# Kernel optimization log

Measured on AMD Instinct MI355X. Metric: run time of the kernel, lower is better.

The kernel has to match this reference:

```python
import jax, jax.numpy as jnp
import numpy as np

B, T, C = 2, 2048, 1024
N_HEAD = 16
HEAD_DIM = C // N_HEAD


def setup_inputs() -> dict:
    key = jax.random.key(0)
    k1, k2, k3 = jax.random.split(key, 3)
    x = jax.random.normal(k1, (B, T, C), dtype=jnp.float32)
    # weights stored as [in, out]; torch Linear computes x @ W.T with weight [out, in]
    W_qkv = jax.random.normal(k2, (C, 3 * C), dtype=jnp.float32) * (1.0 / np.sqrt(C))
    W_proj = jax.random.normal(k3, (C, C), dtype=jnp.float32) * (1.0 / np.sqrt(C))
    return {"x": x, "W_qkv": W_qkv, "W_proj": W_proj}


def reference(x, W_qkv, W_proj):
    Bb, Tt, Cc = x.shape
    qkv = x @ W_qkv                                # [B,T,3C]
    q, k, v = jnp.split(qkv, 3, axis=2)
    # [B,T,H,D] -> [B,H,T,D]
    q = q.reshape(Bb, Tt, N_HEAD, HEAD_DIM).transpose(0, 2, 1, 3)
    k = k.reshape(Bb, Tt, N_HEAD, HEAD_DIM).transpose(0, 2, 1, 3)
    v = v.reshape(Bb, Tt, N_HEAD, HEAD_DIM).transpose(0, 2, 1, 3)
    scale = 1.0 / np.sqrt(HEAD_DIM).astype(np.float32)
    att = jnp.einsum('bhqd,bhkd->bhqk', q, k) * scale   # [B,H,T,T]
    causal = jnp.tril(jnp.ones((Tt, Tt), dtype=bool))
    att = jnp.where(causal[None, None], att, -jnp.inf)
    att = jax.nn.softmax(att, axis=-1)
    y = jnp.einsum('bhqk,bhkd->bhqd', att, v)           # [B,H,T,D]
    y = y.transpose(0, 2, 1, 3).reshape(Bb, Tt, Cc)
    return y @ W_proj
```

## Files before the change

kernel.cpp:

```cpp
#include <hip/hip_runtime.h>
#include <hip/hip_bf16.h>
#include <math.h>


typedef __bf16 bf16_t;
typedef __bf16 bf16x4 __attribute__((ext_vector_type(4)));
typedef __bf16 bf16x8 __attribute__((ext_vector_type(8)));
typedef float  f32x4  __attribute__((ext_vector_type(4)));

#define MFMA16(a, b, c) __builtin_amdgcn_mfma_f32_16x16x32_bf16((a), (b), (c), 0, 0, 0)

#define Bn 2
#define Tn 2048
#define Cn 1024
#define Hn 16
#define Dn 64
#define C3 3072
#define Mn 4096
#define QKW 2048
#define NEG_BIG (-1e30f)
#define SCL2 0.18033688011112042f
#define M2   17.31234049066756f

__device__ __forceinline__ void gload_lds16(const void* g, void* l) {
    __builtin_amdgcn_global_load_lds(
        (const __attribute__((address_space(1))) unsigned int*)g,
        (__attribute__((address_space(3))) unsigned int*)l, 16, 0, 0);
}

__global__ __launch_bounds__(256) void transpose_cvt(const float* __restrict__ in,
                                                     bf16_t* __restrict__ out,
                                                     int K, int N) {
    __shared__ float tile[32][33];
    int n0 = blockIdx.x * 32, k0 = blockIdx.y * 32;
    int tx = threadIdx.x, ty = threadIdx.y;
#pragma unroll
    for (int i = 0; i < 32; i += 8)
        tile[ty + i][tx] = in[(size_t)(k0 + ty + i) * N + n0 + tx];
    __syncthreads();
#pragma unroll
    for (int i = 0; i < 32; i += 8)
        out[(size_t)(n0 + ty + i) * K + k0 + tx] = (bf16_t)tile[tx][ty + i];
}

__global__ __launch_bounds__(256) void cvt_bf16(const float* __restrict__ in,
                                                bf16_t* __restrict__ out) {
    size_t i = ((size_t)blockIdx.x * 256 + threadIdx.x) * 8;
    f32x4 a = *(const f32x4*)(in + i);
    f32x4 b = *(const f32x4*)(in + i + 4);
    bf16x8 r;
    r[0] = (bf16_t)a[0]; r[1] = (bf16_t)a[1]; r[2] = (bf16_t)a[2]; r[3] = (bf16_t)a[3];
    r[4] = (bf16_t)b[0]; r[5] = (bf16_t)b[1]; r[6] = (bf16_t)b[2]; r[7] = (bf16_t)b[3];
    *(bf16x8*)(out + i) = r;
}

template <typename AT, typename CT, int MODE>
__global__ __launch_bounds__(256) void gemm_m97(const AT* __restrict__ A, int lda,
                                                const bf16_t* __restrict__ BT,
                                                CT* __restrict__ Cout, int ldc, int Kd,
                                                bf16_t* __restrict__ qk,
                                                bf16_t* __restrict__ vT) {
    constexpr bool AF32 = (sizeof(AT) == 4);
    __shared__ AT     As[128 * 32];
    __shared__ bf16_t Bs[128 * 32];

    const int tid = threadIdx.x;
    const int w = tid >> 6, lane = tid & 63;
    const int l16 = lane & 15, quad = lane >> 4;
    const int wm = w & 1, wn = w >> 1;
    const int n0 = blockIdx.x * 128;
    const int m0 = blockIdx.y * 128;

    f32x4 zero = {0.f, 0.f, 0.f, 0.f};
    f32x4 acc[4][4];
#pragma unroll
    for (int mb = 0; mb < 4; mb++)
#pragma unroll
        for (int nb = 0; nb < 4; nb++) acc[mb][nb] = zero;

    for (int k = 0; k < Kd; k += 32) {
        __syncthreads();
        if (AF32) {
#pragma unroll
            for (int j = 0; j < 4; j++) {
                int seg = w * 4 + j;
                int r = seg * 8 + (lane >> 3);
                int cc = (lane & 7) ^ (r & 7);
                const float* g = (const float*)A + (size_t)(m0 + r) * lda + k + cc * 4;
                gload_lds16(g, (char*)As + seg * 1024);
            }
        } else {
#pragma unroll
            for (int j = 0; j < 2; j++) {
                int seg = w * 2 + j;
                int r = seg * 16 + (lane >> 2);
                int cc = (lane & 3) ^ (r & 3);
                const bf16_t* g = (const bf16_t*)A + (size_t)(m0 + r) * lda + k + cc * 8;
                gload_lds16(g, (char*)As + seg * 1024);
            }
        }
#pragma unroll
        for (int j = 0; j < 2; j++) {
            int seg = w * 2 + j;
            int r = seg * 16 + (lane >> 2);
            int cc = (lane & 3) ^ (r & 3);
            const bf16_t* g = BT + (size_t)(n0 + r) * Kd + k + cc * 8;
            gload_lds16(g, (char*)Bs + seg * 1024);
        }
        __syncthreads();

        bf16x8 af[4], bf[4];
#pragma unroll
        for (int mb = 0; mb < 4; mb++) {
            int r = wm * 64 + mb * 16 + l16;
            if (AF32) {
                f32x4 x0 = *(const f32x4*)((const char*)As + (r * 8 + ((quad * 2) ^ (r & 7))) * 16);
                f32x4 x1 = *(const f32x4*)((const char*)As + (r * 8 + ((quad * 2 + 1) ^ (r & 7))) * 16);
                bf16x8 t;
                t[0] = (bf16_t)x0[0]; t[1] = (bf16_t)x0[1]; t[2] = (bf16_t)x0[2]; t[3] = (bf16_t)x0[3];
                t[4] = (bf16_t)x1[0]; t[5] = (bf16_t)x1[1]; t[6] = (bf16_t)x1[2]; t[7] = (bf16_t)x1[3];
                af[mb] = t;
            } else {
                af[mb] = *(const bf16x8*)((const char*)As + (r * 4 + (quad ^ (r & 3))) * 16);
            }
        }
#pragma unroll
        for (int nb = 0; nb < 4; nb++) {
            int r = wn * 64 + nb * 16 + l16;
            bf[nb] = *(const bf16x8*)((const char*)Bs + (r * 4 + (quad ^ (r & 3))) * 16);
        }
#pragma unroll
        for (int mb = 0; mb < 4; mb++)
#pragma unroll
            for (int nb = 0; nb < 4; nb++)
                acc[mb][nb] = MFMA16(af[mb], bf[nb], acc[mb][nb]);
    }

#pragma unroll
    for (int mb = 0; mb < 4; mb++)
#pragma unroll
        for (int nb = 0; nb < 4; nb++) {
            const int col = n0 + wn * 64 + nb * 16 + l16;
            const int row0 = m0 + wm * 64 + mb * 16 + quad * 4;
            if (MODE == 0) {
#pragma unroll
                for (int rr = 0; rr < 4; rr++)
                    Cout[(size_t)(row0 + rr) * ldc + col] = (CT)acc[mb][nb][rr];
            } else {
                if (col < 2048) {
#pragma unroll
                    for (int rr = 0; rr < 4; rr++)
                        qk[(size_t)(row0 + rr) * QKW + col] = (bf16_t)acc[mb][nb][rr];
                } else {
                    int hcol = col - 2048;
                    int bb = row0 >> 11, t0 = row0 & 2047;
                    bf16x4 pv;
#pragma unroll
                    for (int rr = 0; rr < 4; rr++) pv[rr] = (bf16_t)acc[mb][nb][rr];
                    *(bf16x4*)(vT + ((size_t)(bb * 1024 + hcol)) * Tn + t0) = pv;
                }
            }
        }
}

__global__ __launch_bounds__(256) void gemm_s(const bf16_t* __restrict__ A, int lda,
                                              const bf16_t* __restrict__ BT,
                                              float* __restrict__ Cout, int ldc, int Kd) {
    __shared__ bf16_t As[64 * 32];
    __shared__ bf16_t Bs[128 * 32];

    const int tid = threadIdx.x;
    const int w = tid >> 6, lane = tid & 63;
    const int l16 = lane & 15, quad = lane >> 4;
    const int wm = w & 1, wn = w >> 1;
    const int n0 = blockIdx.x * 128;
    const int m0 = blockIdx.y * 64;

    f32x4 zero = {0.f, 0.f, 0.f, 0.f};
    f32x4 acc[2][4];
#pragma unroll
    for (int mb = 0; mb < 2; mb++)
#pragma unroll
        for (int nb = 0; nb < 4; nb++) acc[mb][nb] = zero;

    for (int k = 0; k < Kd; k += 32) {
        __syncthreads();
        {
            int r = w * 16 + (lane >> 2);
            int cc = (lane & 3) ^ (r & 3);
            const bf16_t* g = A + (size_t)(m0 + r) * lda + k + cc * 8;
            gload_lds16(g, (char*)As + w * 1024);
        }
#pragma unroll
        for (int j = 0; j < 2; j++) {
            int seg = w * 2 + j;
            int r = seg * 16 + (lane >> 2);
            int cc = (lane & 3) ^ (r & 3);
            const bf16_t* g = BT + (size_t)(n0 + r) * Kd + k + cc * 8;
            gload_lds16(g, (char*)Bs + seg * 1024);
        }
        __syncthreads();

        bf16x8 af[2], bf[4];
#pragma unroll
        for (int mb = 0; mb < 2; mb++) {
            int r = wm * 32 + mb * 16 + l16;
            af[mb] = *(const bf16x8*)((const char*)As + (r * 4 + (quad ^ (r & 3))) * 16);
        }
#pragma unroll
        for (int nb = 0; nb < 4; nb++) {
            int r = wn * 64 + nb * 16 + l16;
            bf[nb] = *(const bf16x8*)((const char*)Bs + (r * 4 + (quad ^ (r & 3))) * 16);
        }
#pragma unroll
        for (int mb = 0; mb < 2; mb++)
#pragma unroll
            for (int nb = 0; nb < 4; nb++)
                acc[mb][nb] = MFMA16(af[mb], bf[nb], acc[mb][nb]);
    }

#pragma unroll
    for (int mb = 0; mb < 2; mb++)
#pragma unroll
        for (int nb = 0; nb < 4; nb++) {
            const int col = n0 + wn * 64 + nb * 16 + l16;
            const int row0 = m0 + wm * 32 + mb * 16 + quad * 4;
#pragma unroll
            for (int rr = 0; rr < 4; rr++)
                Cout[(size_t)(row0 + rr) * ldc + col] = acc[mb][nb][rr];
        }
}

__global__ __launch_bounds__(256) void attn_kernel(bf16_t* __restrict__ qk,
                                                   const bf16_t* __restrict__ vT) {
    const int id = blockIdx.x;
    const int bh = id & 31;
    const int pr = id >> 5;
    const int b = bh >> 4, h = bh & 15;
    const int tA = pr;
    const int tB = 31 - pr;
    const int tmax = tB;

    const int tid = threadIdx.x;
    const int wave = tid >> 6, lane = tid & 63;
    const int l16 = lane & 15, quad = lane >> 4;

    __shared__ bf16_t Kb[2][64 * 64];
    __shared__ bf16_t Vb[2][64 * 64];
    __shared__ bf16_t Pl[4][32][72];

    bf16_t* qbase = qk + (size_t)b * Tn * QKW + h * Dn;
    const bf16_t* kbase = qk + (size_t)b * Tn * QKW + Cn + h * Dn;
    const bf16_t* vbase = vT + (size_t)(b * 1024 + h * Dn) * Tn;

    const int qA = tA * 64 + wave * 16;
    const int qB = tB * 64 + wave * 16;

    bf16x8 qfA[2], qfB[2];
#pragma unroll
    for (int ks = 0; ks < 2; ks++) {
        qfA[ks] = *(const bf16x8*)(qbase + (size_t)(qA + l16) * QKW + ks * 32 + quad * 8);
        qfB[ks] = *(const bf16x8*)(qbase + (size_t)(qB + l16) * QKW + ks * 32 + quad * 8);
    }

    bf16x8 ones;
#pragma unroll
    for (int j = 0; j < 8; j++) ones[j] = (bf16_t)1.0f;

    f32x4 zero = {0.f, 0.f, 0.f, 0.f};
    f32x4 oA[4], oB[4];
    f32x4 olA, olB;
#pragma unroll
    for (int i = 0; i < 4; i++) { oA[i] = zero; oB[i] = zero; }
    olA = zero; olB = zero;

    const int r8 = lane >> 3;
    const int cc = (lane & 7) ^ r8;
    auto STAGE = [&](int t, int pg) {
        const int key0 = t * 64;
#pragma unroll
        for (int j = 0; j < 2; j++) {
            int seg = wave * 2 + j;
            gload_lds16(kbase + (size_t)(key0 + seg * 8 + r8) * QKW + cc * 8,
                        (char*)&Kb[pg][0] + seg * 1024);
            gload_lds16(vbase + (size_t)(seg * 8 + r8) * Tn + key0 + cc * 8,
                        (char*)&Vb[pg][0] + seg * 1024);
        }
    };

    STAGE(0, 0);
    int cur = 0;

    for (int t = 0; t <= tmax; ++t) {
        __syncthreads();
        if (t < tmax) STAGE(t + 1, cur ^ 1);

        const bool shp = (t <= tA);
        const char* Kc = (const char*)&Kb[cur][0];
        const char* Vc = (const char*)&Vb[cur][0];

        bf16x8 kf[2][4];
#pragma unroll
        for (int ks = 0; ks < 2; ks++)
#pragma unroll
            for (int nbk = 0; nbk < 4; nbk++) {
                int R = nbk * 16 + l16;
                kf[ks][nbk] = *(const bf16x8*)(Kc + R * 128 +
                                               (((ks * 4 + quad) ^ (R & 7)) << 4));
            }

        {
            f32x4 s[4];
#pragma unroll
            for (int nbk = 0; nbk < 4; nbk++) s[nbk] = zero;
            __builtin_amdgcn_s_setprio(1);
#pragma unroll
            for (int nbk = 0; nbk < 4; nbk++) {
                s[nbk] = MFMA16(kf[0][nbk], qfB[0], s[nbk]);
                s[nbk] = MFMA16(kf[1][nbk], qfB[1], s[nbk]);
            }
            __builtin_amdgcn_s_setprio(0);
            if (t == tB) {
                int q = qB + l16;
#pragma unroll
                for (int nbk = 0; nbk < 4; nbk++)
#pragma unroll
                    for (int r = 0; r < 4; r++) {
                        int key = t * 64 + nbk * 16 + quad * 4 + r;
                        if (key > q) s[nbk][r] = NEG_BIG;
                    }
            }
#pragma unroll
            for (int nbk = 0; nbk < 4; nbk++) {
                bf16x4 pk;
#pragma unroll
                for (int r = 0; r < 4; r++)
                    pk[r] = (bf16_t)__builtin_exp2f(__builtin_fmaf(s[nbk][r], SCL2, -M2));
                *(bf16x4*)(&Pl[wave][16 + l16][nbk * 16 + quad * 4]) = pk;
            }
        }

        if (shp) {
            f32x4 s[4];
#pragma unroll
            for (int nbk = 0; nbk < 4; nbk++) s[nbk] = zero;
            __builtin_amdgcn_s_setprio(1);
#pragma unroll
            for (int nbk = 0; nbk < 4; nbk++) {
                s[nbk] = MFMA16(kf[0][nbk], qfA[0], s[nbk]);
                s[nbk] = MFMA16(kf[1][nbk], qfA[1], s[nbk]);
            }
            __builtin_amdgcn_s_setprio(0);
            if (t == tA) {
                int q = qA + l16;
#pragma unroll
                for (int nbk = 0; nbk < 4; nbk++)
#pragma unroll
                    for (int r = 0; r < 4; r++) {
                        int key = t * 64 + nbk * 16 + quad * 4 + r;
                        if (key > q) s[nbk][r] = NEG_BIG;
                    }
            }
#pragma unroll
            for (int nbk = 0; nbk < 4; nbk++) {
                bf16x4 pk;
#pragma unroll
                for (int r = 0; r < 4; r++)
                    pk[r] = (bf16_t)__builtin_exp2f(__builtin_fmaf(s[nbk][r], SCL2, -M2));
                *(bf16x4*)(&Pl[wave][l16][nbk * 16 + quad * 4]) = pk;
            }
        }

        bf16x8 pfB[2], pfA[2];
#pragma unroll
        for (int ks = 0; ks < 2; ks++)
            pfB[ks] = *(const bf16x8*)(&Pl[wave][16 + l16][ks * 32 + quad * 8]);
        if (shp) {
#pragma unroll
            for (int ks = 0; ks < 2; ks++)
                pfA[ks] = *(const bf16x8*)(&Pl[wave][l16][ks * 32 + quad * 8]);
        }

        __builtin_amdgcn_s_setprio(1);
#pragma unroll
        for (int ks = 0; ks < 2; ks++) {
#pragma unroll
            for (int nbd = 0; nbd < 4; nbd++) {
                int R = nbd * 16 + l16;
                bf16x8 vf = *(const bf16x8*)(Vc + R * 128 +
                                             (((ks * 4 + quad) ^ (R & 7)) << 4));
                oB[nbd] = MFMA16(pfB[ks], vf, oB[nbd]);
                if (shp) oA[nbd] = MFMA16(pfA[ks], vf, oA[nbd]);
            }
            olB = MFMA16(pfB[ks], ones, olB);
            if (shp) olA = MFMA16(pfA[ks], ones, olA);
        }
        __builtin_amdgcn_s_setprio(0);

        cur ^= 1;
    }

#pragma unroll
    for (int nbd = 0; nbd < 4; nbd++)
#pragma unroll
        for (int r = 0; r < 4; r++) {
            int ta = qA + quad * 4 + r;
            int tb = qB + quad * 4 + r;
            qbase[(size_t)ta * QKW + nbd * 16 + l16] = (bf16_t)(oA[nbd][r] / olA[r]);
            qbase[(size_t)tb * QKW + nbd * 16 + l16] = (bf16_t)(oB[nbd][r] / olB[r]);
        }
}

extern "C" void kernel_launch(void* const* d_in, const int* in_sizes, int n_in,
                              void* d_out, int out_size, void* d_ws, size_t ws_size,
                              hipStream_t stream) {
    const float* x     = (const float*)d_in[0];
    const float* Wqkv  = (const float*)d_in[1];
    const float* Wproj = (const float*)d_in[2];
    float* out = (float*)d_out;

    bf16_t* qk     = (bf16_t*)d_ws;
    bf16_t* vT     = qk + (size_t)Mn * QKW;
    bf16_t* wqkvT  = vT + (size_t)QKW * Tn;
    bf16_t* wprojT = wqkvT + (size_t)C3 * Cn;
    bf16_t* xb     = wprojT + (size_t)Cn * Cn;

    const size_t NEED_XB = ((size_t)Mn * QKW + (size_t)QKW * Tn + (size_t)C3 * Cn +
                            (size_t)Cn * Cn + (size_t)Mn * Cn) * sizeof(bf16_t);

    transpose_cvt<<<dim3(C3 / 32, Cn / 32), dim3(32, 8), 0, stream>>>(Wqkv, wqkvT, Cn, C3);
    transpose_cvt<<<dim3(Cn / 32, Cn / 32), dim3(32, 8), 0, stream>>>(Wproj, wprojT, Cn, Cn);

    if (ws_size >= NEED_XB) {
        cvt_bf16<<<dim3((Mn * Cn) / 2048), 256, 0, stream>>>(x, xb);
        gemm_m97<bf16_t, bf16_t, 1><<<dim3(C3 / 128, Mn / 128), 256, 0, stream>>>(
            xb, Cn, wqkvT, (bf16_t*)nullptr, 0, Cn, qk, vT);
    } else {
        gemm_m97<float, bf16_t, 1><<<dim3(C3 / 128, Mn / 128), 256, 0, stream>>>(
            x, Cn, wqkvT, (bf16_t*)nullptr, 0, Cn, qk, vT);
    }
    attn_kernel<<<dim3(512), 256, 0, stream>>>(qk, vT);
    gemm_s<<<dim3(Cn / 128, Mn / 64), 256, 0, stream>>>(qk, QKW, wprojT, out, Cn, Cn);
}
```

Measured before the change: 193.5 us.

## Keep softmax probabilities in registers by permuting V fragment k-order

Removes the LDS round-trip for the probability tile (write to Pl, then reread as MFMA A-operand). The S accumulator layout is reused directly as the PV A-operand, and the V fragments are read in a matching permuted k-order as two 8-byte halves. This saves LDS traffic and the shared buffer at the cost of twice as many, narrower V reads from LDS. The A-side probabilities are zero-filled when that tile is inactive.

```diff
diff --git a/kernel.cpp b/kernel.cpp
--- a/kernel.cpp
+++ b/kernel.cpp
@@ -28,6 +28,13 @@
         (__attribute__((address_space(3))) unsigned int*)l, 16, 0, 0);
 }
 
+__device__ __forceinline__ bf16x8 cat44(bf16x4 a, bf16x4 b) {
+    bf16x8 r;
+    r[0] = a[0]; r[1] = a[1]; r[2] = a[2]; r[3] = a[3];
+    r[4] = b[0]; r[5] = b[1]; r[6] = b[2]; r[7] = b[3];
+    return r;
+}
+
 __global__ __launch_bounds__(256) void transpose_cvt(const float* __restrict__ in,
                                                      bf16_t* __restrict__ out,
                                                      int K, int N) {
@@ -247,7 +254,6 @@
 
     __shared__ bf16_t Kb[2][64 * 64];
     __shared__ bf16_t Vb[2][64 * 64];
-    __shared__ bf16_t Pl[4][32][72];
 
     bf16_t* qbase = qk + (size_t)b * Tn * QKW + h * Dn;
     const bf16_t* kbase = qk + (size_t)b * Tn * QKW + Cn + h * Dn;
@@ -309,6 +315,8 @@
                                                (((ks * 4 + quad) ^ (R & 7)) << 4));
             }
 
+        bf16x4 pkA[4], pkB[4];
+
         {
             f32x4 s[4];
 #pragma unroll
@@ -331,13 +339,10 @@
                     }
             }
 #pragma unroll
-            for (int nbk = 0; nbk < 4; nbk++) {
-                bf16x4 pk;
+            for (int nbk = 0; nbk < 4; nbk++)
 #pragma unroll
                 for (int r = 0; r < 4; r++)
-                    pk[r] = (bf16_t)__builtin_exp2f(__builtin_fmaf(s[nbk][r], SCL2, -M2));
-                *(bf16x4*)(&Pl[wave][16 + l16][nbk * 16 + quad * 4]) = pk;
-            }
+                    pkB[nbk][r] = (bf16_t)__builtin_exp2f(__builtin_fmaf(s[nbk][r], SCL2, -M2));
         }
 
         if (shp) {
@@ -362,38 +367,35 @@
                     }
             }
 #pragma unroll
-            for (int nbk = 0; nbk < 4; nbk++) {
-                bf16x4 pk;
+            for (int nbk = 0; nbk < 4; nbk++)
 #pragma unroll
                 for (int r = 0; r < 4; r++)
-                    pk[r] = (bf16_t)__builtin_exp2f(__builtin_fmaf(s[nbk][r], SCL2, -M2));
-                *(bf16x4*)(&Pl[wave][l16][nbk * 16 + quad * 4]) = pk;
-            }
-        }
-
-        bf16x8 pfB[2], pfA[2];
-#pragma unroll
-        for (int ks = 0; ks < 2; ks++)
-            pfB[ks] = *(const bf16x8*)(&Pl[wave][16 + l16][ks * 32 + quad * 8]);
-        if (shp) {
-#pragma unroll
-            for (int ks = 0; ks < 2; ks++)
-                pfA[ks] = *(const bf16x8*)(&Pl[wave][l16][ks * 32 + quad * 8]);
-        }
-
+                    pkA[nbk][r] = (bf16_t)__builtin_exp2f(__builtin_fmaf(s[nbk][r], SCL2, -M2));
+        } else {
+#pragma unroll
+            for (int nbk = 0; nbk < 4; nbk++)
+#pragma unroll
+                for (int r = 0; r < 4; r++) pkA[nbk][r] = (bf16_t)0.0f;
+        }
+
+        const int gl = quad >> 1, sub = (quad & 1) * 8;
         __builtin_amdgcn_s_setprio(1);
 #pragma unroll
         for (int ks = 0; ks < 2; ks++) {
+            bf16x8 pfB_ = cat44(pkB[2 * ks], pkB[2 * ks + 1]);
+            bf16x8 pfA_ = cat44(pkA[2 * ks], pkA[2 * ks + 1]);
 #pragma unroll
             for (int nbd = 0; nbd < 4; nbd++) {
-                int R = nbd * 16 + l16;
-                bf16x8 vf = *(const bf16x8*)(Vc + R * 128 +
-                                             (((ks * 4 + quad) ^ (R & 7)) << 4));
-                oB[nbd] = MFMA16(pfB[ks], vf, oB[nbd]);
-                if (shp) oA[nbd] = MFMA16(pfA[ks], vf, oA[nbd]);
-            }
-            olB = MFMA16(pfB[ks], ones, olB);
-            if (shp) olA = MFMA16(pfA[ks], ones, olA);
+                int R = nbd * 16 + l16, r7 = R & 7;
+                const char* row = Vc + R * 128;
+                bf16x4 lo = *(const bf16x4*)(row + (((ks * 4 + gl) ^ r7) << 4) + sub);
+                bf16x4 hi = *(const bf16x4*)(row + (((ks * 4 + 2 + gl) ^ r7) << 4) + sub);
+                bf16x8 vf = cat44(lo, hi);
+                oB[nbd] = MFMA16(pfB_, vf, oB[nbd]);
+                if (shp) oA[nbd] = MFMA16(pfA_, vf, oA[nbd]);
+            }
+            olB = MFMA16(pfB_, ones, olB);
+            if (shp) olA = MFMA16(pfA_, ones, olA);
         }
         __builtin_amdgcn_s_setprio(0);
 
```

Result: no change. 192.9 us (-0.3%).
